# Kernel tuning notes

Hardware: AMD Instinct MI355X
Metric: run time of the kernel (lower is better)

Reference implementation:

```python
import jax, jax.numpy as jnp
import numpy as np

VOCAB, EMB, H, LAYERS, B, T = 50000, 128, 128, 3, 64, 512


def _lstm_dir(x, w_ih, w_hh, b_ih, b_hh, h0, c0, reverse):
    # x: [B,T,Din]; w_ih: [4H,Din]; w_hh: [4H,H]; h0,c0: [B,H]
    xg = jnp.einsum('btd,gd->btg', x, w_ih) + b_ih + b_hh  # [B,T,4H]

    def step(carry, xg_t):
        h, c = carry
        g = xg_t + h @ w_hh.T  # [B,4H]
        i, f, gg, o = jnp.split(g, 4, axis=-1)  # torch gate order i,f,g,o
        c = jax.nn.sigmoid(f) * c + jax.nn.sigmoid(i) * jnp.tanh(gg)
        h = jax.nn.sigmoid(o) * jnp.tanh(c)
        return (h, c), h

    _, hs = jax.lax.scan(step, (h0, c0), jnp.swapaxes(xg, 0, 1), reverse=reverse)
    return jnp.swapaxes(hs, 0, 1)  # [B,T,H], aligned with input time order


def _bidir_layer(x, w_ih, w_hh, b_ih, b_hh, h0, c0):
    # stacked params: leading dim 2 = (fwd, bwd)
    fwd = _lstm_dir(x, w_ih[0], w_hh[0], b_ih[0], b_hh[0], h0[0], c0[0], False)
    bwd = _lstm_dir(x, w_ih[1], w_hh[1], b_ih[1], b_hh[1], h0[1], c0[1], True)
    return jnp.concatenate([fwd, bwd], axis=-1)  # [B,T,2H]


def setup_inputs() -> dict:
    key = jax.random.key(0)
    ks = jax.random.split(key, 20)
    s = 1.0 / np.sqrt(H)
    inp = {
        'X_batch': jax.random.randint(ks[0], (B, T), 0, VOCAB),
        'emb': jax.random.normal(ks[1], (VOCAB, EMB), jnp.float32),
        'hx': jax.random.normal(ks[2], (2 * LAYERS, B, H), jnp.float32),
        'cx': jax.random.normal(ks[3], (2 * LAYERS, B, H), jnp.float32),
        'lin_w': jax.random.uniform(ks[4], (1, 2 * H), jnp.float32, -s, s),
        'lin_b': jax.random.uniform(ks[5], (1,), jnp.float32, -s, s),
    }
    k = 6
    for l in range(LAYERS):
        din = EMB if l == 0 else 2 * H
        inp[f'w_ih_{l}'] = jax.random.uniform(ks[k], (2, 4 * H, din), jnp.float32, -s, s); k += 1
        inp[f'w_hh_{l}'] = jax.random.uniform(ks[k], (2, 4 * H, H), jnp.float32, -s, s); k += 1
        inp[f'b_ih_{l}'] = jax.random.uniform(ks[k], (2, 4 * H), jnp.float32, -s, s); k += 1
        inp[f'b_hh_{l}'] = jax.random.uniform(ks[k], (2, 4 * H), jnp.float32, -s, s); k += 1
    return inp


def reference(X_batch, emb, hx, cx, lin_w, lin_b,
              w_ih_0, w_hh_0, b_ih_0, b_hh_0,
              w_ih_1, w_hh_1, b_ih_1, b_hh_1,
              w_ih_2, w_hh_2, b_ih_2, b_hh_2):
    x = emb[X_batch]  # [B,T,EMB]
    params = [(w_ih_0, w_hh_0, b_ih_0, b_hh_0),
              (w_ih_1, w_hh_1, b_ih_1, b_hh_1),
              (w_ih_2, w_hh_2, b_ih_2, b_hh_2)]
    for l, (wi, wh, bi, bh) in enumerate(params):
        x = _bidir_layer(x, wi, wh, bi, bh, hx[2 * l:2 * l + 2], cx[2 * l:2 * l + 2])
    # linear head applied to last timestep (== output[:, -1] of full linear)
    return x[:, -1] @ lin_w.T + lin_b  # [B,1]
```

## Files before the change

kernel.cpp:

```cpp
#include <hip/hip_runtime.h>
#include <hip/hip_bf16.h>
#include <stdint.h>

#define B_    64
#define T_    512
#define EMB_  128
#define H_    128
#define G4    512
#define M_    (B_ * T_)

typedef __attribute__((ext_vector_type(8))) short     short8;
typedef __attribute__((ext_vector_type(4))) float     floatx4;
typedef __attribute__((ext_vector_type(2))) _Float16  half2v;

#define GLDS(g, l) __builtin_amdgcn_global_load_lds( \
    (__attribute__((address_space(1))) void*)(g),    \
    (__attribute__((address_space(3))) void*)(l), 16, 0, 0)

__device__ __forceinline__ unsigned short f2bf_bits(float f) {
  __hip_bfloat16 h = __float2bfloat16(f);
  return *reinterpret_cast<unsigned short*>(&h);
}
__device__ __forceinline__ float bf_bits2f(unsigned short u) {
  unsigned int x = ((unsigned int)u) << 16;
  return __uint_as_float(x);
}
__device__ __forceinline__ float sigm(float x) {
  return __fdividef(1.0f, 1.0f + __expf(-x));
}
__device__ __forceinline__ float tanh_fast(float x) {
  return 1.0f - __fdividef(2.0f, __expf(2.0f * x) + 1.0f);
}

__device__ __forceinline__ unsigned int pack_f16x2(float a, float b) {
  half2v h; h.x = (_Float16)a; h.y = (_Float16)b;
  return __builtin_bit_cast(unsigned int, h);
}
__device__ __forceinline__ half2v u2h2(unsigned int u) {
  return __builtin_bit_cast(half2v, u);
}

#if __has_builtin(__builtin_amdgcn_fdot2)
__device__ __forceinline__ float fdot2(half2v a, half2v b, float c) {
  return __builtin_amdgcn_fdot2(a, b, c, false);
}
#else
__device__ __forceinline__ float fdot2(half2v a, half2v b, float c) {
  return fmaf((float)a.x, (float)b.x, fmaf((float)a.y, (float)b.y, c));
}
#endif

__device__ __forceinline__ float pair_bfly_add(float x) {
  return x + __int_as_float(
      __builtin_amdgcn_mov_dpp(__float_as_int(x), 0xB1, 0xF, 0xF, true));
}

__device__ __forceinline__ void barrier_lds_only() {
  __builtin_amdgcn_s_waitcnt(0xC07F);
  __builtin_amdgcn_s_barrier();
}

__device__ __forceinline__ void  store_xg(float* p, float v)  { *p = v; }
__device__ __forceinline__ void  store_xg(unsigned short* p, float v) { *p = f2bf_bits(v); }
__device__ __forceinline__ float load_xg(const float* p)  { return *p; }
__device__ __forceinline__ float load_xg(const unsigned short* p) { return bf_bits2f(*p); }

__global__ void k_gather(const int* __restrict__ X, const float* __restrict__ emb,
                         unsigned short* __restrict__ x0) {
  int i = blockIdx.x * 256 + threadIdx.x;
  int row = i >> 5, c4 = i & 31;
  float4 v = ((const float4*)emb)[(size_t)X[row] * 32 + c4];
  ushort4 o;
  o.x = f2bf_bits(v.x); o.y = f2bf_bits(v.y); o.z = f2bf_bits(v.z); o.w = f2bf_bits(v.w);
  ((ushort4*)x0)[i] = o;
}

__global__ void k_prep(const float* __restrict__ w, const float* __restrict__ bi,
                       const float* __restrict__ bh, unsigned short* __restrict__ wb,
                       float* __restrict__ bias, int nw) {
  int i = blockIdx.x * blockDim.x + threadIdx.x;
  int stride = gridDim.x * blockDim.x;
  for (int k = i; k < nw; k += stride) wb[k] = f2bf_bits(w[k]);
  for (int k = i; k < 2 * G4; k += stride) bias[k] = bi[k] + bh[k];
}

__global__ void k_prep_whh(const float* __restrict__ Whh, unsigned int* __restrict__ wf) {
  int i = blockIdx.x * 256 + threadIdx.x;
  int dir = i >> 15;
  int r   = i & 0x7FFF;
  int i4  = r >> 10;
  int r2  = r & 0x3FF;
  int ts  = r2 >> 2;
  int q   = r2 & 3;
  int d   = i4 * 4 + q;
  int g   = d >> 5;
  int jj  = d & 31;
  int lane = ts & 63, w = ts >> 6;
  int p = lane & 1, ul = lane >> 1;
  int u = w * 32 + ul;
  int k = 64 * p + 2 * jj;
  const float* wr = Whh + ((size_t)dir * G4 + g * H_ + u) * H_ + k;
  wf[i] = pack_f16x2(wr[0], wr[1]);
}

template <typename XG_T>
__global__ __launch_bounds__(256, 2) void k_gemm(
    const unsigned short* __restrict__ A,
    const unsigned short* __restrict__ W,
    const float* __restrict__ bias,
    XG_T* __restrict__ xg,
    int K) {
  __shared__ unsigned short sA[128 * 32];
  __shared__ unsigned short sB[128 * 32];
  const int tid  = threadIdx.x;
  const int lane = tid & 63;
  const int wave = tid >> 6;
  const int mt = blockIdx.x, nt = blockIdx.y, dir = blockIdx.z;
  const size_t Arow0 = (size_t)mt * 128;
  const int    Ncol0 = nt * 128;
  const unsigned short* Wd = W + (size_t)dir * G4 * K;

  const int srow = tid >> 2;
  const int qlog = (tid & 3) ^ ((tid >> 4) & 3);
  auto ldsA0 = (__attribute__((address_space(3))) void*)(sA + wave * 512);
  auto ldsA1 = (__attribute__((address_space(3))) void*)(sA + 2048 + wave * 512);
  auto ldsB0 = (__attribute__((address_space(3))) void*)(sB + wave * 512);
  auto ldsB1 = (__attribute__((address_space(3))) void*)(sB + 2048 + wave * 512);

  floatx4 acc[4][4];
#pragma unroll
  for (int i = 0; i < 4; ++i)
#pragma unroll
    for (int j = 0; j < 4; ++j) acc[i][j] = (floatx4)0.0f;

  const int wrow = (wave >> 1) * 64, wcol = (wave & 1) * 64;
  const int frow = lane & 15;
  const int fq   = lane >> 4;

  for (int kt = 0; kt < K; kt += 32) {
    const unsigned short* gA0 = A  + (Arow0 + srow) * (size_t)K + kt + qlog * 8;
    const unsigned short* gB0 = Wd + (size_t)(Ncol0 + srow) * K + kt + qlog * 8;
    GLDS(gA0, ldsA0);
    GLDS(gA0 + (size_t)64 * K, ldsA1);
    GLDS(gB0, ldsB0);
    GLDS(gB0 + (size_t)64 * K, ldsB1);
    __syncthreads();

    short8 af[4], bf[4];
#pragma unroll
    for (int i = 0; i < 4; ++i) {
      int r  = wrow + 16 * i + frow;
      int rn = wcol + 16 * i + frow;
      af[i] = *(const short8*)(sA + r  * 32 + ((fq ^ ((r  >> 2) & 3)) * 8));
      bf[i] = *(const short8*)(sB + rn * 32 + ((fq ^ ((rn >> 2) & 3)) * 8));
    }
#pragma unroll
    for (int i = 0; i < 4; ++i)
#pragma unroll
      for (int j = 0; j < 4; ++j)
        acc[i][j] = __builtin_amdgcn_mfma_f32_16x16x32_bf16(af[i], bf[j], acc[i][j], 0, 0, 0);
    __syncthreads();
  }

  const int r0 = (lane >> 4) * 4;
  const int cc = lane & 15;
  XG_T* xgd = xg + (size_t)dir * M_ * G4;
#pragma unroll
  for (int j = 0; j < 4; ++j) {
    int gcol = Ncol0 + wcol + 16 * j + cc;
    float bs = bias[dir * G4 + gcol];
#pragma unroll
    for (int i = 0; i < 4; ++i) {
      size_t rowb = Arow0 + wrow + 16 * i + r0;
#pragma unroll
      for (int r = 0; r < 4; ++r)
        store_xg(&xgd[(rowb + r) * G4 + gcol], acc[i][j][r] + bs);
    }
  }
}

template <typename XG_T>
__global__ __attribute__((amdgpu_flat_work_group_size(256, 256),
                          amdgpu_waves_per_eu(1, 1))) void k_scan(
    const unsigned int* __restrict__ wf,
    const float* __restrict__ hx0,
    const float* __restrict__ cx0,
    const XG_T* __restrict__ xg,
    unsigned short* __restrict__ y)
{
  const int b   = blockIdx.x & 63;
  const int dir = blockIdx.x >> 6;
  const int tid = threadIdx.x;
  const int lane = tid & 63;
  const int wave = tid >> 6;
  const int p  = lane & 1;
  const int ul = lane >> 1;
  const int u  = wave * 32 + ul;

  __shared__ __align__(16) unsigned short h16[2][128];

  uint4 wv[32];
  const uint4* wfv = (const uint4*)wf;
#pragma unroll
  for (int i = 0; i < 32; ++i) wv[i] = wfv[(dir * 32 + i) * 256 + tid];

  float c = cx0[(size_t)dir * B_ * H_ + b * H_ + u];
  if (p == 0) {
    float h0 = hx0[(size_t)dir * B_ * H_ + b * H_ + u];
    h16[0][u] = (unsigned short)(pack_f16x2(h0, 0.0f) & 0xFFFF);
  }

  const XG_T* xgb = xg + ((size_t)dir * M_ + (size_t)b * T_) * G4;
  const intptr_t xstep = dir ? -(intptr_t)G4 : (intptr_t)G4;
  const int o0 = (2 * p) * H_ + u;
  const int o1 = o0 + H_;
  const XG_T* xrow0 = xgb + (dir ? (size_t)(T_ - 1) * G4 : 0);
  float xa0 = load_xg(xrow0 + o0), xb0 = load_xg(xrow0 + o1);
  float xa1 = load_xg(xrow0 + xstep + o0), xb1 = load_xg(xrow0 + xstep + o1);
  const XG_T* xld = xrow0 + 2 * xstep;

  unsigned short* yp = y + ((size_t)b * T_ + (dir ? T_ - 1 : 0)) * (2 * H_)
                         + dir * H_ + u;
  const intptr_t ystep = dir ? -(intptr_t)(2 * H_) : (intptr_t)(2 * H_);

  __syncthreads();

  auto dots = [&](int par, float xva, float xvb,
                  float& g0, float& g1, float& g2, float& g3) {
    const uint4* hv4 = (const uint4*)&h16[par][0];
    uint4 hq[8];
#pragma unroll
    for (int i = 0; i < 8; ++i) hq[i] = hv4[8 * p + i];
    half2v hh[32];
#pragma unroll
    for (int i = 0; i < 8; ++i) {
      hh[4 * i + 0] = u2h2(hq[i].x);
      hh[4 * i + 1] = u2h2(hq[i].y);
      hh[4 * i + 2] = u2h2(hq[i].z);
      hh[4 * i + 3] = u2h2(hq[i].w);
    }
    float A0 = 0, B0 = 0, A1 = 0, B1 = 0, A2 = 0, B2 = 0, A3 = 0, B3 = 0;
#pragma unroll
    for (int j = 0; j < 16; ++j) {
      int d0 = j, d1 = j + 16;
      A0 = fdot2(u2h2(((const unsigned int*)&wv[(0 * 32 + d0) >> 2])[(0 * 32 + d0) & 3]), hh[d0], A0);
      A1 = fdot2(u2h2(((const unsigned int*)&wv[(1 * 32 + d0) >> 2])[(1 * 32 + d0) & 3]), hh[d0], A1);
      A2 = fdot2(u2h2(((const unsigned int*)&wv[(2 * 32 + d0) >> 2])[(2 * 32 + d0) & 3]), hh[d0], A2);
      A3 = fdot2(u2h2(((const unsigned int*)&wv[(3 * 32 + d0) >> 2])[(3 * 32 + d0) & 3]), hh[d0], A3);
      B0 = fdot2(u2h2(((const unsigned int*)&wv[(0 * 32 + d1) >> 2])[(0 * 32 + d1) & 3]), hh[d1], B0);
      B1 = fdot2(u2h2(((const unsigned int*)&wv[(1 * 32 + d1) >> 2])[(1 * 32 + d1) & 3]), hh[d1], B1);
      B2 = fdot2(u2h2(((const unsigned int*)&wv[(2 * 32 + d1) >> 2])[(2 * 32 + d1) & 3]), hh[d1], B2);
      B3 = fdot2(u2h2(((const unsigned int*)&wv[(3 * 32 + d1) >> 2])[(3 * 32 + d1) & 3]), hh[d1], B3);
    }
    g0 = A0 + B0; g1 = A1 + B1; g2 = A2 + B2; g3 = A3 + B3;
    g0 += (p == 0) ? xva : 0.0f;
    g1 += (p == 0) ? xvb : 0.0f;
    g2 += (p == 1) ? xva : 0.0f;
    g3 += (p == 1) ? xvb : 0.0f;
  };

  auto finish = [&](int par, float g0, float g1, float g2, float g3) {
    g0 = pair_bfly_add(g0);
    g1 = pair_bfly_add(g1);
    g2 = pair_bfly_add(g2);
    g3 = pair_bfly_add(g3);
    float iv = sigm(g0), fv = sigm(g1), gv = tanh_fast(g2), ov = sigm(g3);
    c = fmaf(fv, c, iv * gv);
    float h = ov * tanh_fast(c);
    if (p == 0) {
      h16[par ^ 1][u] = (unsigned short)(pack_f16x2(h, 0.0f) & 0xFFFF);
      *yp = f2bf_bits(h);
    }
    yp += ystep;
    barrier_lds_only();
  };

  for (int t = 0; t < T_; t += 2) {
    {
      float va = xa0, vb = xb0;
      if (t + 2 < T_) { xa0 = load_xg(xld + o0); xb0 = load_xg(xld + o1); }
      else            { xa0 = 0.0f; xb0 = 0.0f; }
      xld += xstep;
      float a0, a1, a2, a3;
      dots(0, va, vb, a0, a1, a2, a3);
      finish(0, a0, a1, a2, a3);
    }
    {
      float va = xa1, vb = xb1;
      if (t + 3 < T_) { xa1 = load_xg(xld + o0); xb1 = load_xg(xld + o1); }
      else            { xa1 = 0.0f; xb1 = 0.0f; }
      xld += xstep;
      float a0, a1, a2, a3;
      dots(1, va, vb, a0, a1, a2, a3);
      finish(1, a0, a1, a2, a3);
    }
  }
}

__global__ void k_head(const unsigned short* __restrict__ y2, const float* __restrict__ lw,
                       const float* __restrict__ lb, float* __restrict__ out) {
  int b = blockIdx.x, l = threadIdx.x;
  const unsigned short* row = y2 + ((size_t)b * T_ + (T_ - 1)) * (2 * H_);
  float s = 0;
#pragma unroll
  for (int k = 0; k < 4; ++k) s += bf_bits2f(row[l + 64 * k]) * lw[l + 64 * k];
#pragma unroll
  for (int off = 32; off > 0; off >>= 1) s += __shfl_down(s, off);
  if (l == 0) out[b] = s + lb[0];
}

template <typename XG_T>
static inline void run_layers(const unsigned int* const* wfs,
                              const unsigned short* x0,
                              unsigned short* y0, unsigned short* y1, unsigned short* y2,
                              const unsigned short* wb0, const unsigned short* wb1,
                              const unsigned short* wb2,
                              const float* bias0, const float* bias1, const float* bias2,
                              const float* hx, const float* cx,
                              XG_T* xg, hipStream_t stream) {
  dim3 gg(M_ / 128, G4 / 128, 2);
  k_gemm<XG_T><<<gg, 256, 0, stream>>>(x0, wb0, bias0, xg, EMB_);
  k_scan<XG_T><<<128, 256, 0, stream>>>(wfs[0], hx, cx, xg, y0);
  k_gemm<XG_T><<<gg, 256, 0, stream>>>(y0, wb1, bias1, xg, 2 * H_);
  k_scan<XG_T><<<128, 256, 0, stream>>>(wfs[1], hx + 2 * B_ * H_, cx + 2 * B_ * H_, xg, y1);
  k_gemm<XG_T><<<gg, 256, 0, stream>>>(y1, wb2, bias2, xg, 2 * H_);
  k_scan<XG_T><<<128, 256, 0, stream>>>(wfs[2], hx + 4 * B_ * H_, cx + 4 * B_ * H_, xg, y2);
}

extern "C" void kernel_launch(void* const* d_in, const int* in_sizes, int n_in,
                              void* d_out, int out_size, void* d_ws, size_t ws_size,
                              hipStream_t stream) {
  const int*   X   = (const int*)d_in[0];
  const float* emb = (const float*)d_in[1];
  const float* hx  = (const float*)d_in[2];
  const float* cx  = (const float*)d_in[3];
  const float* lw  = (const float*)d_in[4];
  const float* lb  = (const float*)d_in[5];
  const float* w_ih[3] = {(const float*)d_in[6],  (const float*)d_in[10], (const float*)d_in[14]};
  const float* w_hh[3] = {(const float*)d_in[7],  (const float*)d_in[11], (const float*)d_in[15]};
  const float* b_ih[3] = {(const float*)d_in[8],  (const float*)d_in[12], (const float*)d_in[16]};
  const float* b_hh[3] = {(const float*)d_in[9],  (const float*)d_in[13], (const float*)d_in[17]};
  float* out = (float*)d_out;

  char* ws = (char*)d_ws;
  size_t off = 0;
  auto carve = [&](size_t bytes) {
    char* p = ws + off;
    off = (off + bytes + 255) & ~(size_t)255;
    return p;
  };
  unsigned short* x0  = (unsigned short*)carve((size_t)M_ * EMB_ * 2);
  unsigned short* y0  = (unsigned short*)carve((size_t)M_ * 2 * H_ * 2);
  unsigned short* y1  = (unsigned short*)carve((size_t)M_ * 2 * H_ * 2);
  unsigned short* y2  = (unsigned short*)carve((size_t)M_ * 2 * H_ * 2);
  unsigned short* wb0 = (unsigned short*)carve((size_t)2 * G4 * EMB_ * 2);
  unsigned short* wb1 = (unsigned short*)carve((size_t)2 * G4 * 2 * H_ * 2);
  unsigned short* wb2 = (unsigned short*)carve((size_t)2 * G4 * 2 * H_ * 2);
  float* bias0 = (float*)carve(2 * G4 * 4);
  float* bias1 = (float*)carve(2 * G4 * 4);
  float* bias2 = (float*)carve(2 * G4 * 4);
  unsigned int* wf0 = (unsigned int*)carve((size_t)65536 * 4);
  unsigned int* wf1 = (unsigned int*)carve((size_t)65536 * 4);
  unsigned int* wf2 = (unsigned int*)carve((size_t)65536 * 4);
  const size_t xg_f32_bytes = (size_t)2 * M_ * G4 * 4;
  const bool use_f32 = (off + xg_f32_bytes) <= ws_size;
  void* xg = carve(use_f32 ? xg_f32_bytes : xg_f32_bytes / 2);

  k_prep<<<256, 256, 0, stream>>>(w_ih[0], b_ih[0], b_hh[0], wb0, bias0, 2 * G4 * EMB_);
  k_prep<<<256, 256, 0, stream>>>(w_ih[1], b_ih[1], b_hh[1], wb1, bias1, 2 * G4 * 2 * H_);
  k_prep<<<256, 256, 0, stream>>>(w_ih[2], b_ih[2], b_hh[2], wb2, bias2, 2 * G4 * 2 * H_);
  k_prep_whh<<<256, 256, 0, stream>>>(w_hh[0], wf0);
  k_prep_whh<<<256, 256, 0, stream>>>(w_hh[1], wf1);
  k_prep_whh<<<256, 256, 0, stream>>>(w_hh[2], wf2);
  k_gather<<<(M_ * 32) / 256, 256, 0, stream>>>(X, emb, x0);

  const unsigned int* wfs[3] = {wf0, wf1, wf2};
  if (use_f32)
    run_layers<float>(wfs, x0, y0, y1, y2, wb0, wb1, wb2, bias0, bias1, bias2,
                      hx, cx, (float*)xg, stream);
  else
    run_layers<unsigned short>(wfs, x0, y0, y1, y2, wb0, wb1, wb2, bias0, bias1, bias2,
                               hx, cx, (unsigned short*)xg, stream);

  k_head<<<64, 64, 0, stream>>>(y2, lw, lb, out);
}
```

Before: 1.114 ms.

## Process two batch sequences per scan block to interleave recurrences

Each scan block now carries two independent batch sequences, with separate LDS hidden-state buffers and cell states. Their dot products and gate updates are interleaved so one sequence's work can cover the other's latency, and both share a single barrier per step. The grid shrinks from 128 to 64 blocks, and the end-of-sequence bounds checks on the xg prefetch are removed, so the last steps read past the current sequence's rows. On a GPU with many CUs this serialises twice the work on each block's per-step critical path, which the overlap may not make up for.

```diff
diff --git a/kernel.cpp b/kernel.cpp
--- a/kernel.cpp
+++ b/kernel.cpp
@@ -188,8 +188,10 @@
     const XG_T* __restrict__ xg,
     unsigned short* __restrict__ y)
 {
-  const int b   = blockIdx.x & 63;
-  const int dir = blockIdx.x >> 6;
+  const int dir = blockIdx.x >> 5;
+  const int bp  = blockIdx.x & 31;
+  const int bA  = 2 * bp;
+  const int bB  = 2 * bp + 1;
   const int tid = threadIdx.x;
   const int lane = tid & 63;
   const int wave = tid >> 6;
@@ -197,40 +199,47 @@
   const int ul = lane >> 1;
   const int u  = wave * 32 + ul;
 
-  __shared__ __align__(16) unsigned short h16[2][128];
+  __shared__ __align__(16) unsigned short h16[2][2][128];
 
   uint4 wv[32];
   const uint4* wfv = (const uint4*)wf;
 #pragma unroll
   for (int i = 0; i < 32; ++i) wv[i] = wfv[(dir * 32 + i) * 256 + tid];
 
-  float c = cx0[(size_t)dir * B_ * H_ + b * H_ + u];
+  float cA = cx0[(size_t)dir * B_ * H_ + bA * H_ + u];
+  float cB = cx0[(size_t)dir * B_ * H_ + bB * H_ + u];
   if (p == 0) {
-    float h0 = hx0[(size_t)dir * B_ * H_ + b * H_ + u];
-    h16[0][u] = (unsigned short)(pack_f16x2(h0, 0.0f) & 0xFFFF);
+    float hA0 = hx0[(size_t)dir * B_ * H_ + bA * H_ + u];
+    float hB0 = hx0[(size_t)dir * B_ * H_ + bB * H_ + u];
+    h16[0][0][u] = (unsigned short)(pack_f16x2(hA0, 0.0f) & 0xFFFF);
+    h16[1][0][u] = (unsigned short)(pack_f16x2(hB0, 0.0f) & 0xFFFF);
   }
 
-  const XG_T* xgb = xg + ((size_t)dir * M_ + (size_t)b * T_) * G4;
   const intptr_t xstep = dir ? -(intptr_t)G4 : (intptr_t)G4;
   const int o0 = (2 * p) * H_ + u;
   const int o1 = o0 + H_;
-  const XG_T* xrow0 = xgb + (dir ? (size_t)(T_ - 1) * G4 : 0);
-  float xa0 = load_xg(xrow0 + o0), xb0 = load_xg(xrow0 + o1);
-  float xa1 = load_xg(xrow0 + xstep + o0), xb1 = load_xg(xrow0 + xstep + o1);
-  const XG_T* xld = xrow0 + 2 * xstep;
-
-  unsigned short* yp = y + ((size_t)b * T_ + (dir ? T_ - 1 : 0)) * (2 * H_)
-                         + dir * H_ + u;
+
+  const XG_T* xgbA = xg + ((size_t)dir * M_ + (size_t)bA * T_) * G4;
+  const XG_T* xgbB = xg + ((size_t)dir * M_ + (size_t)bB * T_) * G4;
+  const XG_T* xrowA = xgbA + (dir ? (size_t)(T_ - 1) * G4 : 0);
+  const XG_T* xrowB = xgbB + (dir ? (size_t)(T_ - 1) * G4 : 0);
+  float xaA0 = load_xg(xrowA + o0), xbA0 = load_xg(xrowA + o1);
+  float xaA1 = load_xg(xrowA + xstep + o0), xbA1 = load_xg(xrowA + xstep + o1);
+  float xaB0 = load_xg(xrowB + o0), xbB0 = load_xg(xrowB + o1);
+  float xaB1 = load_xg(xrowB + xstep + o0), xbB1 = load_xg(xrowB + xstep + o1);
+  const XG_T* xldA = xrowA + 2 * xstep;
+  const XG_T* xldB = xrowB + 2 * xstep;
+
+  unsigned short* ypA = y + ((size_t)bA * T_ + (dir ? T_ - 1 : 0)) * (2 * H_)
+                          + dir * H_ + u;
+  unsigned short* ypB = y + ((size_t)bB * T_ + (dir ? T_ - 1 : 0)) * (2 * H_)
+                          + dir * H_ + u;
   const intptr_t ystep = dir ? -(intptr_t)(2 * H_) : (intptr_t)(2 * H_);
 
   __syncthreads();
 
-  auto dots = [&](int par, float xva, float xvb,
-                  float& g0, float& g1, float& g2, float& g3) {
-    const uint4* hv4 = (const uint4*)&h16[par][0];
-    uint4 hq[8];
-#pragma unroll
-    for (int i = 0; i < 8; ++i) hq[i] = hv4[8 * p + i];
+  auto dot = [&](const uint4 (&hq)[8], float xva, float xvb,
+                 float& g0, float& g1, float& g2, float& g3) {
     half2v hh[32];
 #pragma unroll
     for (int i = 0; i < 8; ++i) {
@@ -259,7 +268,8 @@
     g3 += (p == 1) ? xvb : 0.0f;
   };
 
-  auto finish = [&](int par, float g0, float g1, float g2, float g3) {
+  auto finish = [&](int seq, int par, float g0, float g1, float g2, float g3,
+                    float& c, unsigned short*& yp) {
     g0 = pair_bfly_add(g0);
     g1 = pair_bfly_add(g1);
     g2 = pair_bfly_add(g2);
@@ -268,32 +278,45 @@
     c = fmaf(fv, c, iv * gv);
     float h = ov * tanh_fast(c);
     if (p == 0) {
-      h16[par ^ 1][u] = (unsigned short)(pack_f16x2(h, 0.0f) & 0xFFFF);
+      h16[seq][par ^ 1][u] = (unsigned short)(pack_f16x2(h, 0.0f) & 0xFFFF);
       *yp = f2bf_bits(h);
     }
     yp += ystep;
+  };
+
+  auto phase = [&](int par, float& xaA, float& xbA, float& xaB, float& xbB) {
+    uint4 hqA[8];
+    {
+      const uint4* hv4 = (const uint4*)&h16[0][par][0];
+#pragma unroll
+      for (int i = 0; i < 8; ++i) hqA[i] = hv4[8 * p + i];
+    }
+    float vaA = xaA, vbA = xbA;
+    xaA = load_xg(xldA + o0); xbA = load_xg(xldA + o1);
+    xldA += xstep;
+    float a0, a1, a2, a3;
+    dot(hqA, vaA, vbA, a0, a1, a2, a3);
+
+    uint4 hqB[8];
+    {
+      const uint4* hv4 = (const uint4*)&h16[1][par][0];
+#pragma unroll
+      for (int i = 0; i < 8; ++i) hqB[i] = hv4[8 * p + i];
+    }
+    float vaB = xaB, vbB = xbB;
+    xaB = load_xg(xldB + o0); xbB = load_xg(xldB + o1);
+    xldB += xstep;
+
+    finish(0, par, a0, a1, a2, a3, cA, ypA);
+    float b0, b1, b2, b3;
+    dot(hqB, vaB, vbB, b0, b1, b2, b3);
+    finish(1, par, b0, b1, b2, b3, cB, ypB);
     barrier_lds_only();
   };
 
   for (int t = 0; t < T_; t += 2) {
-    {
-      float va = xa0, vb = xb0;
-      if (t + 2 < T_) { xa0 = load_xg(xld + o0); xb0 = load_xg(xld + o1); }
-      else            { xa0 = 0.0f; xb0 = 0.0f; }
-      xld += xstep;
-      float a0, a1, a2, a3;
-      dots(0, va, vb, a0, a1, a2, a3);
-      finish(0, a0, a1, a2, a3);
-    }
-    {
-      float va = xa1, vb = xb1;
-      if (t + 3 < T_) { xa1 = load_xg(xld + o0); xb1 = load_xg(xld + o1); }
-      else            { xa1 = 0.0f; xb1 = 0.0f; }
-      xld += xstep;
-      float a0, a1, a2, a3;
-      dots(1, va, vb, a0, a1, a2, a3);
-      finish(1, a0, a1, a2, a3);
-    }
+    phase(0, xaA0, xbA0, xaB0, xbB0);
+    phase(1, xaA1, xbA1, xaB1, xbB1);
   }
 }
 
@@ -320,11 +343,11 @@
                               XG_T* xg, hipStream_t stream) {
   dim3 gg(M_ / 128, G4 / 128, 2);
   k_gemm<XG_T><<<gg, 256, 0, stream>>>(x0, wb0, bias0, xg, EMB_);
-  k_scan<XG_T><<<128, 256, 0, stream>>>(wfs[0], hx, cx, xg, y0);
+  k_scan<XG_T><<<64, 256, 0, stream>>>(wfs[0], hx, cx, xg, y0);
   k_gemm<XG_T><<<gg, 256, 0, stream>>>(y0, wb1, bias1, xg, 2 * H_);
-  k_scan<XG_T><<<128, 256, 0, stream>>>(wfs[1], hx + 2 * B_ * H_, cx + 2 * B_ * H_, xg, y1);
+  k_scan<XG_T><<<64, 256, 0, stream>>>(wfs[1], hx + 2 * B_ * H_, cx + 2 * B_ * H_, xg, y1);
   k_gemm<XG_T><<<gg, 256, 0, stream>>>(y1, wb2, bias2, xg, 2 * H_);
-  k_scan<XG_T><<<128, 256, 0, stream>>>(wfs[2], hx + 4 * B_ * H_, cx + 4 * B_ * H_, xg, y2);
+  k_scan<XG_T><<<64, 256, 0, stream>>>(wfs[2], hx + 4 * B_ * H_, cx + 4 * B_ * H_, xg, y2);
 }
 
 extern "C" void kernel_launch(void* const* d_in, const int* in_sizes, int n_in,
```

Result: slower. 1.956 ms (+75.5%).

## Batch LSTM recurrence over 16 sequences per block using f16 MFMA

Applied to the files above, without the earlier changes.

Rewrites the recurrent scan so each 512-thread block handles 16 batch rows of one direction. The hidden-state matvec becomes 16x16x32 f16 MFMA tiles, with W_hh held in registers in a new fragment layout and h kept in swizzled LDS. This replaces the per-sequence fdot2-and-butterfly scheme that used 128 blocks. The xg buffer is now always bf16, dropping the f32 path to halve its traffic. The catch is only 8 blocks run on the GPU, so per-step latency depends on MFMA chain depth and barriers across 8 waves.

```diff
diff --git a/kernel.cpp b/kernel.cpp
--- a/kernel.cpp
+++ b/kernel.cpp
@@ -12,6 +12,7 @@
 typedef __attribute__((ext_vector_type(8))) short     short8;
 typedef __attribute__((ext_vector_type(4))) float     floatx4;
 typedef __attribute__((ext_vector_type(2))) _Float16  half2v;
+typedef __attribute__((ext_vector_type(8))) _Float16  half8;
 
 #define GLDS(g, l) __builtin_amdgcn_global_load_lds( \
     (__attribute__((address_space(1))) void*)(g),    \
@@ -31,39 +32,15 @@
 __device__ __forceinline__ float tanh_fast(float x) {
   return 1.0f - __fdividef(2.0f, __expf(2.0f * x) + 1.0f);
 }
-
 __device__ __forceinline__ unsigned int pack_f16x2(float a, float b) {
   half2v h; h.x = (_Float16)a; h.y = (_Float16)b;
   return __builtin_bit_cast(unsigned int, h);
 }
-__device__ __forceinline__ half2v u2h2(unsigned int u) {
-  return __builtin_bit_cast(half2v, u);
-}
-
-#if __has_builtin(__builtin_amdgcn_fdot2)
-__device__ __forceinline__ float fdot2(half2v a, half2v b, float c) {
-  return __builtin_amdgcn_fdot2(a, b, c, false);
-}
-#else
-__device__ __forceinline__ float fdot2(half2v a, half2v b, float c) {
-  return fmaf((float)a.x, (float)b.x, fmaf((float)a.y, (float)b.y, c));
-}
-#endif
-
-__device__ __forceinline__ float pair_bfly_add(float x) {
-  return x + __int_as_float(
-      __builtin_amdgcn_mov_dpp(__float_as_int(x), 0xB1, 0xF, 0xF, true));
-}
 
 __device__ __forceinline__ void barrier_lds_only() {
   __builtin_amdgcn_s_waitcnt(0xC07F);
   __builtin_amdgcn_s_barrier();
 }
-
-__device__ __forceinline__ void  store_xg(float* p, float v)  { *p = v; }
-__device__ __forceinline__ void  store_xg(unsigned short* p, float v) { *p = f2bf_bits(v); }
-__device__ __forceinline__ float load_xg(const float* p)  { return *p; }
-__device__ __forceinline__ float load_xg(const unsigned short* p) { return bf_bits2f(*p); }
 
 __global__ void k_gather(const int* __restrict__ X, const float* __restrict__ emb,
                          unsigned short* __restrict__ x0) {
@@ -86,29 +63,23 @@
 
 __global__ void k_prep_whh(const float* __restrict__ Whh, unsigned int* __restrict__ wf) {
   int i = blockIdx.x * 256 + threadIdx.x;
-  int dir = i >> 15;
-  int r   = i & 0x7FFF;
-  int i4  = r >> 10;
-  int r2  = r & 0x3FF;
-  int ts  = r2 >> 2;
-  int q   = r2 & 3;
-  int d   = i4 * 4 + q;
-  int g   = d >> 5;
-  int jj  = d & 31;
-  int lane = ts & 63, w = ts >> 6;
-  int p = lane & 1, ul = lane >> 1;
-  int u = w * 32 + ul;
-  int k = 64 * p + 2 * jj;
-  const float* wr = Whh + ((size_t)dir * G4 + g * H_ + u) * H_ + k;
+  int jp  = i & 3;
+  int l   = (i >> 2) & 63;
+  int kk  = (i >> 8) & 3;
+  int g   = (i >> 10) & 3;
+  int w   = (i >> 12) & 7;
+  int dir = (i >> 15) & 1;
+  int row = g * 128 + w * 16 + (l & 15);
+  int k0  = kk * 32 + (l >> 4) * 8 + 2 * jp;
+  const float* wr = Whh + ((size_t)dir * G4 + row) * H_ + k0;
   wf[i] = pack_f16x2(wr[0], wr[1]);
 }
 
-template <typename XG_T>
 __global__ __launch_bounds__(256, 2) void k_gemm(
     const unsigned short* __restrict__ A,
     const unsigned short* __restrict__ W,
     const float* __restrict__ bias,
-    XG_T* __restrict__ xg,
+    unsigned short* __restrict__ xg,
     int K) {
   __shared__ unsigned short sA[128 * 32];
   __shared__ unsigned short sB[128 * 32];
@@ -164,7 +135,7 @@
 
   const int r0 = (lane >> 4) * 4;
   const int cc = lane & 15;
-  XG_T* xgd = xg + (size_t)dir * M_ * G4;
+  unsigned short* xgd = xg + (size_t)dir * M_ * G4;
 #pragma unroll
   for (int j = 0; j < 4; ++j) {
     int gcol = Ncol0 + wcol + 16 * j + cc;
@@ -174,126 +145,149 @@
       size_t rowb = Arow0 + wrow + 16 * i + r0;
 #pragma unroll
       for (int r = 0; r < 4; ++r)
-        store_xg(&xgd[(rowb + r) * G4 + gcol], acc[i][j][r] + bs);
+        xgd[(rowb + r) * G4 + gcol] = f2bf_bits(acc[i][j][r] + bs);
     }
   }
 }
 
-template <typename XG_T>
-__global__ __attribute__((amdgpu_flat_work_group_size(256, 256),
-                          amdgpu_waves_per_eu(1, 1))) void k_scan(
+__global__ __launch_bounds__(512, 2) void k_scan(
     const unsigned int* __restrict__ wf,
     const float* __restrict__ hx0,
     const float* __restrict__ cx0,
-    const XG_T* __restrict__ xg,
+    const unsigned short* __restrict__ xg,
     unsigned short* __restrict__ y)
 {
-  const int b   = blockIdx.x & 63;
-  const int dir = blockIdx.x >> 6;
-  const int tid = threadIdx.x;
+  const int dir = blockIdx.x >> 2;
+  const int b0  = (blockIdx.x & 3) * 16;
+  const int tid  = threadIdx.x;
   const int lane = tid & 63;
-  const int wave = tid >> 6;
-  const int p  = lane & 1;
-  const int ul = lane >> 1;
-  const int u  = wave * 32 + ul;
-
-  __shared__ __align__(16) unsigned short h16[2][128];
-
-  uint4 wv[32];
-  const uint4* wfv = (const uint4*)wf;
-#pragma unroll
-  for (int i = 0; i < 32; ++i) wv[i] = wfv[(dir * 32 + i) * 256 + tid];
-
-  float c = cx0[(size_t)dir * B_ * H_ + b * H_ + u];
-  if (p == 0) {
-    float h0 = hx0[(size_t)dir * B_ * H_ + b * H_ + u];
-    h16[0][u] = (unsigned short)(pack_f16x2(h0, 0.0f) & 0xFFFF);
-  }
-
-  const XG_T* xgb = xg + ((size_t)dir * M_ + (size_t)b * T_) * G4;
-  const intptr_t xstep = dir ? -(intptr_t)G4 : (intptr_t)G4;
-  const int o0 = (2 * p) * H_ + u;
-  const int o1 = o0 + H_;
-  const XG_T* xrow0 = xgb + (dir ? (size_t)(T_ - 1) * G4 : 0);
-  float xa0 = load_xg(xrow0 + o0), xb0 = load_xg(xrow0 + o1);
-  float xa1 = load_xg(xrow0 + xstep + o0), xb1 = load_xg(xrow0 + xstep + o1);
-  const XG_T* xld = xrow0 + 2 * xstep;
-
-  unsigned short* yp = y + ((size_t)b * T_ + (dir ? T_ - 1 : 0)) * (2 * H_)
-                         + dir * H_ + u;
-  const intptr_t ystep = dir ? -(intptr_t)(2 * H_) : (intptr_t)(2 * H_);
+  const int w    = tid >> 6;
+  const int lq   = lane >> 4;
+  const int cc   = lane & 15;
+  const int u    = 16 * w + cc;
+
+  __shared__ __align__(16) unsigned short Hs[2][16 * 128];
+
+  half8 wB[4][4];
+  {
+    const uint4* wv = (const uint4*)wf;
+    const int base = (dir * 8 + w) * 16;
+#pragma unroll
+    for (int g = 0; g < 4; ++g)
+#pragma unroll
+      for (int kk = 0; kk < 4; ++kk)
+        wB[g][kk] = __builtin_bit_cast(half8, wv[(base + g * 4 + kk) * 64 + lane]);
+  }
+
+  float c[4];
+#pragma unroll
+  for (int r = 0; r < 4; ++r)
+    c[r] = cx0[(size_t)dir * B_ * H_ + (b0 + lq * 4 + r) * H_ + u];
+
+  {
+    int row = tid >> 5;
+    int c0  = (tid & 31) * 4;
+    const float* hp = hx0 + (size_t)dir * B_ * H_ + (b0 + row) * H_ + c0;
+    float4 hv = *(const float4*)hp;
+    uint2 pk;
+    pk.x = pack_f16x2(hv.x, hv.y);
+    pk.y = pack_f16x2(hv.z, hv.w);
+    int byteoff = (row * 256 + c0 * 2) ^ ((row & 7) << 4);
+    *(uint2*)((char*)&Hs[0][0] + byteoff) = pk;
+  }
+
+  int aoff[4];
+#pragma unroll
+  for (int kk = 0; kk < 4; ++kk)
+    aoff[kk] = (cc * 256 + kk * 64 + lq * 16) ^ ((cc & 7) << 4);
+
+  int hwidx[4];
+#pragma unroll
+  for (int r = 0; r < 4; ++r) {
+    int row = lq * 4 + r;
+    hwidx[r] = ((row * 256 + u * 2) ^ ((row & 7) << 4)) >> 1;
+  }
+
+  const unsigned short* xgd = xg + (size_t)dir * M_ * G4;
+  int xofs[4][4];
+#pragma unroll
+  for (int g = 0; g < 4; ++g)
+#pragma unroll
+    for (int r = 0; r < 4; ++r)
+      xofs[g][r] = (b0 + lq * 4 + r) * (T_ * G4) + g * H_ + u;
+
+  int yofs[4];
+#pragma unroll
+  for (int r = 0; r < 4; ++r)
+    yofs[r] = (b0 + lq * 4 + r) * (T_ * 2 * H_) + dir * H_ + u;
+
+  const int td = dir ? -1 : 1;
+  int t0 = dir ? (T_ - 1) : 0;
+
+  unsigned short xpA[4][4], xpB[4][4];
+  {
+    const unsigned short* p0 = xgd + (intptr_t)t0 * G4;
+    const unsigned short* p1 = xgd + (intptr_t)(t0 + td) * G4;
+#pragma unroll
+    for (int g = 0; g < 4; ++g)
+#pragma unroll
+      for (int r = 0; r < 4; ++r) {
+        xpA[g][r] = p0[xofs[g][r]];
+        xpB[g][r] = p1[xofs[g][r]];
+      }
+  }
 
   __syncthreads();
 
-  auto dots = [&](int par, float xva, float xvb,
-                  float& g0, float& g1, float& g2, float& g3) {
-    const uint4* hv4 = (const uint4*)&h16[par][0];
-    uint4 hq[8];
-#pragma unroll
-    for (int i = 0; i < 8; ++i) hq[i] = hv4[8 * p + i];
-    half2v hh[32];
-#pragma unroll
-    for (int i = 0; i < 8; ++i) {
-      hh[4 * i + 0] = u2h2(hq[i].x);
-      hh[4 * i + 1] = u2h2(hq[i].y);
-      hh[4 * i + 2] = u2h2(hq[i].z);
-      hh[4 * i + 3] = u2h2(hq[i].w);
+  auto step = [&](int par, int tcur, unsigned short (&xp)[4][4]) {
+    half8 a[4];
+#pragma unroll
+    for (int kk = 0; kk < 4; ++kk)
+      a[kk] = __builtin_bit_cast(half8,
+          *(const uint4*)((const char*)&Hs[par][0] + aoff[kk]));
+    floatx4 ac[4];
+#pragma unroll
+    for (int g = 0; g < 4; ++g) ac[g] = (floatx4)0.0f;
+#pragma unroll
+    for (int kk = 0; kk < 4; ++kk)
+#pragma unroll
+      for (int g = 0; g < 4; ++g)
+        ac[g] = __builtin_amdgcn_mfma_f32_16x16x32_f16(a[kk], wB[g][kk], ac[g], 0, 0, 0);
+
+    float xv[4][4];
+#pragma unroll
+    for (int g = 0; g < 4; ++g)
+#pragma unroll
+      for (int r = 0; r < 4; ++r) xv[g][r] = bf_bits2f(xp[g][r]);
+    {
+      const unsigned short* pn = xgd + (intptr_t)(tcur + 2 * td) * G4;
+#pragma unroll
+      for (int g = 0; g < 4; ++g)
+#pragma unroll
+        for (int r = 0; r < 4; ++r) xp[g][r] = pn[xofs[g][r]];
     }
-    float A0 = 0, B0 = 0, A1 = 0, B1 = 0, A2 = 0, B2 = 0, A3 = 0, B3 = 0;
-#pragma unroll
-    for (int j = 0; j < 16; ++j) {
-      int d0 = j, d1 = j + 16;
-      A0 = fdot2(u2h2(((const unsigned int*)&wv[(0 * 32 + d0) >> 2])[(0 * 32 + d0) & 3]), hh[d0], A0);
-      A1 = fdot2(u2h2(((const unsigned int*)&wv[(1 * 32 + d0) >> 2])[(1 * 32 + d0) & 3]), hh[d0], A1);
-      A2 = fdot2(u2h2(((const unsigned int*)&wv[(2 * 32 + d0) >> 2])[(2 * 32 + d0) & 3]), hh[d0], A2);
-      A3 = fdot2(u2h2(((const unsigned int*)&wv[(3 * 32 + d0) >> 2])[(3 * 32 + d0) & 3]), hh[d0], A3);
-      B0 = fdot2(u2h2(((const unsigned int*)&wv[(0 * 32 + d1) >> 2])[(0 * 32 + d1) & 3]), hh[d1], B0);
-      B1 = fdot2(u2h2(((const unsigned int*)&wv[(1 * 32 + d1) >> 2])[(1 * 32 + d1) & 3]), hh[d1], B1);
-      B2 = fdot2(u2h2(((const unsigned int*)&wv[(2 * 32 + d1) >> 2])[(2 * 32 + d1) & 3]), hh[d1], B2);
-      B3 = fdot2(u2h2(((const unsigned int*)&wv[(3 * 32 + d1) >> 2])[(3 * 32 + d1) & 3]), hh[d1], B3);
+
+    unsigned short* ydst = y + (size_t)tcur * (2 * H_);
+    unsigned short* hdst = &Hs[par ^ 1][0];
+#pragma unroll
+    for (int r = 0; r < 4; ++r) {
+      float gi = ac[0][r] + xv[0][r];
+      float gf = ac[1][r] + xv[1][r];
+      float gg = ac[2][r] + xv[2][r];
+      float go = ac[3][r] + xv[3][r];
+      float iv = sigm(gi), fv = sigm(gf), gv = tanh_fast(gg), ov = sigm(go);
+      c[r] = fmaf(fv, c[r], iv * gv);
+      float h = ov * tanh_fast(c[r]);
+      hdst[hwidx[r]] = (unsigned short)(pack_f16x2(h, 0.0f) & 0xFFFF);
+      ydst[yofs[r]] = f2bf_bits(h);
     }
-    g0 = A0 + B0; g1 = A1 + B1; g2 = A2 + B2; g3 = A3 + B3;
-    g0 += (p == 0) ? xva : 0.0f;
-    g1 += (p == 0) ? xvb : 0.0f;
-    g2 += (p == 1) ? xva : 0.0f;
-    g3 += (p == 1) ? xvb : 0.0f;
-  };
-
-  auto finish = [&](int par, float g0, float g1, float g2, float g3) {
-    g0 = pair_bfly_add(g0);
-    g1 = pair_bfly_add(g1);
-    g2 = pair_bfly_add(g2);
-    g3 = pair_bfly_add(g3);
-    float iv = sigm(g0), fv = sigm(g1), gv = tanh_fast(g2), ov = sigm(g3);
-    c = fmaf(fv, c, iv * gv);
-    float h = ov * tanh_fast(c);
-    if (p == 0) {
-      h16[par ^ 1][u] = (unsigned short)(pack_f16x2(h, 0.0f) & 0xFFFF);
-      *yp = f2bf_bits(h);
-    }
-    yp += ystep;
     barrier_lds_only();
   };
 
-  for (int t = 0; t < T_; t += 2) {
-    {
-      float va = xa0, vb = xb0;
-      if (t + 2 < T_) { xa0 = load_xg(xld + o0); xb0 = load_xg(xld + o1); }
-      else            { xa0 = 0.0f; xb0 = 0.0f; }
-      xld += xstep;
-      float a0, a1, a2, a3;
-      dots(0, va, vb, a0, a1, a2, a3);
-      finish(0, a0, a1, a2, a3);
-    }
-    {
-      float va = xa1, vb = xb1;
-      if (t + 3 < T_) { xa1 = load_xg(xld + o0); xb1 = load_xg(xld + o1); }
-      else            { xa1 = 0.0f; xb1 = 0.0f; }
-      xld += xstep;
-      float a0, a1, a2, a3;
-      dots(1, va, vb, a0, a1, a2, a3);
-      finish(1, a0, a1, a2, a3);
-    }
+  for (int it = 0; it < T_; it += 2) {
+    step(0, t0, xpA);
+    step(1, t0 + td, xpB);
+    t0 += 2 * td;
   }
 }
 
@@ -309,7 +303,6 @@
   if (l == 0) out[b] = s + lb[0];
 }
 
-template <typename XG_T>
 static inline void run_layers(const unsigned int* const* wfs,
                               const unsigned short* x0,
                               unsigned short* y0, unsigned short* y1, unsigned short* y2,
@@ -317,14 +310,14 @@
                               const unsigned short* wb2,
                               const float* bias0, const float* bias1, const float* bias2,
                               const float* hx, const float* cx,
-                              XG_T* xg, hipStream_t stream) {
+                              unsigned short* xg, hipStream_t stream) {
   dim3 gg(M_ / 128, G4 / 128, 2);
-  k_gemm<XG_T><<<gg, 256, 0, stream>>>(x0, wb0, bias0, xg, EMB_);
-  k_scan<XG_T><<<128, 256, 0, stream>>>(wfs[0], hx, cx, xg, y0);
-  k_gemm<XG_T><<<gg, 256, 0, stream>>>(y0, wb1, bias1, xg, 2 * H_);
-  k_scan<XG_T><<<128, 256, 0, stream>>>(wfs[1], hx + 2 * B_ * H_, cx + 2 * B_ * H_, xg, y1);
-  k_gemm<XG_T><<<gg, 256, 0, stream>>>(y1, wb2, bias2, xg, 2 * H_);
-  k_scan<XG_T><<<128, 256, 0, stream>>>(wfs[2], hx + 4 * B_ * H_, cx + 4 * B_ * H_, xg, y2);
+  k_gemm<<<gg, 256, 0, stream>>>(x0, wb0, bias0, xg, EMB_);
+  k_scan<<<8, 512, 0, stream>>>(wfs[0], hx, cx, xg, y0);
+  k_gemm<<<gg, 256, 0, stream>>>(y0, wb1, bias1, xg, 2 * H_);
+  k_scan<<<8, 512, 0, stream>>>(wfs[1], hx + 2 * B_ * H_, cx + 2 * B_ * H_, xg, y1);
+  k_gemm<<<gg, 256, 0, stream>>>(y1, wb2, bias2, xg, 2 * H_);
+  k_scan<<<8, 512, 0, stream>>>(wfs[2], hx + 4 * B_ * H_, cx + 4 * B_ * H_, xg, y2);
 }
 
 extern "C" void kernel_launch(void* const* d_in, const int* in_sizes, int n_in,
@@ -362,9 +355,7 @@
   unsigned int* wf0 = (unsigned int*)carve((size_t)65536 * 4);
   unsigned int* wf1 = (unsigned int*)carve((size_t)65536 * 4);
   unsigned int* wf2 = (unsigned int*)carve((size_t)65536 * 4);
-  const size_t xg_f32_bytes = (size_t)2 * M_ * G4 * 4;
-  const bool use_f32 = (off + xg_f32_bytes) <= ws_size;
-  void* xg = carve(use_f32 ? xg_f32_bytes : xg_f32_bytes / 2);
+  unsigned short* xg = (unsigned short*)carve((size_t)2 * M_ * G4 * 2);
 
   k_prep<<<256, 256, 0, stream>>>(w_ih[0], b_ih[0], b_hh[0], wb0, bias0, 2 * G4 * EMB_);
   k_prep<<<256, 256, 0, stream>>>(w_ih[1], b_ih[1], b_hh[1], wb1, bias1, 2 * G4 * 2 * H_);
@@ -375,12 +366,8 @@
   k_gather<<<(M_ * 32) / 256, 256, 0, stream>>>(X, emb, x0);
 
   const unsigned int* wfs[3] = {wf0, wf1, wf2};
-  if (use_f32)
-    run_layers<float>(wfs, x0, y0, y1, y2, wb0, wb1, wb2, bias0, bias1, bias2,
-                      hx, cx, (float*)xg, stream);
-  else
-    run_layers<unsigned short>(wfs, x0, y0, y1, y2, wb0, wb1, wb2, bias0, bias1, bias2,
-                               hx, cx, (unsigned short*)xg, stream);
+  run_layers(wfs, x0, y0, y1, y2, wb0, wb1, wb2, bias0, bias1, bias2,
+             hx, cx, xg, stream);
 
   k_head<<<64, 64, 0, stream>>>(y2, lw, lb, out);
 }
```

Result: slower. 2.691 ms (+141.4%).

## Pair two batch rows per scan block and interleave their dot and gate phases

Applied to the files above, without the earlier changes.

Each scan workgroup now holds two batch sequences as two 256-thread groups sharing one CU. While one group computes the recurrent dot products, the other computes gate activations and writes h, with a barrier between phases, so the two latency-bound phases of independent sequences overlap. This halves the grid to 64 blocks of 512 threads and requires two waves per EU, which doubles register pressure against the large per-thread weight arrays. It also loads the xg prefetch one step past the end of the sequence, which may read out of bounds at the last step.

```diff
diff --git a/kernel.cpp b/kernel.cpp
--- a/kernel.cpp
+++ b/kernel.cpp
@@ -180,34 +180,37 @@
 }
 
 template <typename XG_T>
-__global__ __attribute__((amdgpu_flat_work_group_size(256, 256),
-                          amdgpu_waves_per_eu(1, 1))) void k_scan(
+__global__ __attribute__((amdgpu_flat_work_group_size(512, 512),
+                          amdgpu_waves_per_eu(2, 2))) void k_scan(
     const unsigned int* __restrict__ wf,
     const float* __restrict__ hx0,
     const float* __restrict__ cx0,
     const XG_T* __restrict__ xg,
     unsigned short* __restrict__ y)
 {
-  const int b   = blockIdx.x & 63;
-  const int dir = blockIdx.x >> 6;
+  const int dir = blockIdx.x >> 5;
+  const int bp  = blockIdx.x & 31;
   const int tid = threadIdx.x;
+  const int grp = tid >> 8;
+  const int ts  = tid & 255;
   const int lane = tid & 63;
-  const int wave = tid >> 6;
+  const int w4  = ts >> 6;
   const int p  = lane & 1;
   const int ul = lane >> 1;
-  const int u  = wave * 32 + ul;
+  const int u  = w4 * 32 + ul;
+  const int b  = 2 * bp + grp;
 
   __shared__ __align__(16) unsigned short h16[2][128];
 
   uint4 wv[32];
   const uint4* wfv = (const uint4*)wf;
 #pragma unroll
-  for (int i = 0; i < 32; ++i) wv[i] = wfv[(dir * 32 + i) * 256 + tid];
+  for (int i = 0; i < 32; ++i) wv[i] = wfv[(dir * 32 + i) * 256 + ts];
 
   float c = cx0[(size_t)dir * B_ * H_ + b * H_ + u];
   if (p == 0) {
     float h0 = hx0[(size_t)dir * B_ * H_ + b * H_ + u];
-    h16[0][u] = (unsigned short)(pack_f16x2(h0, 0.0f) & 0xFFFF);
+    h16[grp][u] = (unsigned short)(pack_f16x2(h0, 0.0f) & 0xFFFF);
   }
 
   const XG_T* xgb = xg + ((size_t)dir * M_ + (size_t)b * T_) * G4;
@@ -215,8 +218,8 @@
   const int o0 = (2 * p) * H_ + u;
   const int o1 = o0 + H_;
   const XG_T* xrow0 = xgb + (dir ? (size_t)(T_ - 1) * G4 : 0);
-  float xa0 = load_xg(xrow0 + o0), xb0 = load_xg(xrow0 + o1);
-  float xa1 = load_xg(xrow0 + xstep + o0), xb1 = load_xg(xrow0 + xstep + o1);
+  float xa_c = load_xg(xrow0 + o0),         xb_c = load_xg(xrow0 + o1);
+  float xa_n = load_xg(xrow0 + xstep + o0), xb_n = load_xg(xrow0 + xstep + o1);
   const XG_T* xld = xrow0 + 2 * xstep;
 
   unsigned short* yp = y + ((size_t)b * T_ + (dir ? T_ - 1 : 0)) * (2 * H_)
@@ -225,9 +228,14 @@
 
   __syncthreads();
 
-  auto dots = [&](int par, float xva, float xvb,
-                  float& g0, float& g1, float& g2, float& g3) {
-    const uint4* hv4 = (const uint4*)&h16[par][0];
+  float g0, g1, g2, g3;
+
+  auto dots = [&]() {
+    float xva = xa_c, xvb = xb_c;
+    xa_c = xa_n; xb_c = xb_n;
+    xa_n = load_xg(xld + o0); xb_n = load_xg(xld + o1);
+    xld += xstep;
+    const uint4* hv4 = (const uint4*)&h16[grp][0];
     uint4 hq[8];
 #pragma unroll
     for (int i = 0; i < 8; ++i) hq[i] = hv4[8 * p + i];
@@ -259,42 +267,30 @@
     g3 += (p == 1) ? xvb : 0.0f;
   };
 
-  auto finish = [&](int par, float g0, float g1, float g2, float g3) {
-    g0 = pair_bfly_add(g0);
-    g1 = pair_bfly_add(g1);
-    g2 = pair_bfly_add(g2);
-    g3 = pair_bfly_add(g3);
-    float iv = sigm(g0), fv = sigm(g1), gv = tanh_fast(g2), ov = sigm(g3);
+  auto tail = [&]() {
+    float t0v = pair_bfly_add(g0);
+    float t1v = pair_bfly_add(g1);
+    float t2v = pair_bfly_add(g2);
+    float t3v = pair_bfly_add(g3);
+    float iv = sigm(t0v), fv = sigm(t1v), gv = tanh_fast(t2v), ov = sigm(t3v);
     c = fmaf(fv, c, iv * gv);
     float h = ov * tanh_fast(c);
     if (p == 0) {
-      h16[par ^ 1][u] = (unsigned short)(pack_f16x2(h, 0.0f) & 0xFFFF);
+      h16[grp][u] = (unsigned short)(pack_f16x2(h, 0.0f) & 0xFFFF);
       *yp = f2bf_bits(h);
     }
     yp += ystep;
+  };
+
+  for (int t = 0; t < T_; ++t) {
+    if (grp == 0)      dots();
+    else if (t > 0)    tail();
     barrier_lds_only();
-  };
-
-  for (int t = 0; t < T_; t += 2) {
-    {
-      float va = xa0, vb = xb0;
-      if (t + 2 < T_) { xa0 = load_xg(xld + o0); xb0 = load_xg(xld + o1); }
-      else            { xa0 = 0.0f; xb0 = 0.0f; }
-      xld += xstep;
-      float a0, a1, a2, a3;
-      dots(0, va, vb, a0, a1, a2, a3);
-      finish(0, a0, a1, a2, a3);
-    }
-    {
-      float va = xa1, vb = xb1;
-      if (t + 3 < T_) { xa1 = load_xg(xld + o0); xb1 = load_xg(xld + o1); }
-      else            { xa1 = 0.0f; xb1 = 0.0f; }
-      xld += xstep;
-      float a0, a1, a2, a3;
-      dots(1, va, vb, a0, a1, a2, a3);
-      finish(1, a0, a1, a2, a3);
-    }
+    if (grp == 0)      tail();
+    else               dots();
+    barrier_lds_only();
   }
+  if (grp) tail();
 }
 
 __global__ void k_head(const unsigned short* __restrict__ y2, const float* __restrict__ lw,
@@ -320,11 +316,11 @@
                               XG_T* xg, hipStream_t stream) {
   dim3 gg(M_ / 128, G4 / 128, 2);
   k_gemm<XG_T><<<gg, 256, 0, stream>>>(x0, wb0, bias0, xg, EMB_);
-  k_scan<XG_T><<<128, 256, 0, stream>>>(wfs[0], hx, cx, xg, y0);
+  k_scan<XG_T><<<64, 512, 0, stream>>>(wfs[0], hx, cx, xg, y0);
   k_gemm<XG_T><<<gg, 256, 0, stream>>>(y0, wb1, bias1, xg, 2 * H_);
-  k_scan<XG_T><<<128, 256, 0, stream>>>(wfs[1], hx + 2 * B_ * H_, cx + 2 * B_ * H_, xg, y1);
+  k_scan<XG_T><<<64, 512, 0, stream>>>(wfs[1], hx + 2 * B_ * H_, cx + 2 * B_ * H_, xg, y1);
   k_gemm<XG_T><<<gg, 256, 0, stream>>>(y1, wb2, bias2, xg, 2 * H_);
-  k_scan<XG_T><<<128, 256, 0, stream>>>(wfs[2], hx + 4 * B_ * H_, cx + 4 * B_ * H_, xg, y2);
+  k_scan<XG_T><<<64, 512, 0, stream>>>(wfs[2], hx + 4 * B_ * H_, cx + 4 * B_ * H_, xg, y2);
 }
 
 extern "C" void kernel_launch(void* const* d_in, const int* in_sizes, int n_in,
```

Result: slower. 1.820 ms (+63.3%).
